# Kernel tuning notes

Measured on AMD Instinct MI355X. Metric: run time of the kernel, lower is better.

Reference implementation:

```python
import jax, jax.numpy as jnp
import numpy as np

THRESH = 0.9   # config['thresh_cnn']
R = 2          # config['radius'] -> maxpool kernel 2R+1=5, stride 1, padding R


def setup_inputs() -> dict:
    key = jax.random.key(0)
    # [B=1, C=1, D=64, H=512, W=512]
    pred_vol = jax.random.uniform(key, (1, 1, 64, 512, 512), dtype=jnp.float32)
    return {"pred_vol": pred_vol}


def reference(pred_vol):
    # threshold: keep values > thresh, else 0
    pred_thresh = jnp.where(pred_vol > THRESH, pred_vol, 0.0)
    # 3D max-pool, kernel 2R+1, stride 1, padding R (torch pads with -inf for maxpool)
    k = 2 * R + 1
    mp = jax.lax.reduce_window(
        pred_thresh, -jnp.inf, jax.lax.max,
        window_dimensions=(1, 1, k, k, k),
        window_strides=(1, 1, 1, 1, 1),
        padding=[(0, 0), (0, 0), (R, R), (R, R), (R, R)],
    )
    # keep only strict local maxima of the thresholded volume
    conf_vol = jnp.where((mp > 0.0) & (mp == pred_thresh), mp, 0.0)
    return jnp.squeeze(conf_vol)  # [D, H, W] dense peak confidence map
```

## Files before the change

kernel.cpp:

```cpp
#include <hip/hip_runtime.h>


#define THRESH 0.9f

constexpr int D = 64, H = 512, W = 512;
constexpr int TW = 64;
constexpr int TH = 16;
constexpr int DCHUNK = 16;
constexpr int HALO = 2;
constexpr int LROWS = TH + 2 * HALO;
constexpr int RAWQ  = TW / 4 + 2;
constexpr int RAWQ_S = RAWQ + 1;
constexpr int WMQ   = TW / 4;
constexpr int WMQ_S = WMQ + 1;

__device__ __forceinline__ float4 thresh4(float4 v) {
    v.x = (v.x > THRESH) ? v.x : 0.f;
    v.y = (v.y > THRESH) ? v.y : 0.f;
    v.z = (v.z > THRESH) ? v.z : 0.f;
    v.w = (v.w > THRESH) ? v.w : 0.f;
    return v;
}

__device__ __forceinline__ float4 max4(float4 a, float4 b) {
    return make_float4(fmaxf(a.x, b.x), fmaxf(a.y, b.y),
                       fmaxf(a.z, b.z), fmaxf(a.w, b.w));
}

__device__ __forceinline__ float4 wmax5(float4 a, float4 b, float4 c) {
    const float f2 = a.z, f3 = a.w, f4 = b.x, f5 = b.y, f6 = b.z, f7 = b.w;
    const float f8 = c.x, f9 = c.y;
    const float m45 = fmaxf(f4, f5);
    const float m56 = fmaxf(f5, f6);
    const float m345 = fmaxf(f3, m45);
    const float m456 = fmaxf(f4, m56);
    const float m567 = fmaxf(m56, f7);
    const float m678 = fmaxf(fmaxf(f6, f7), f8);
    float4 r;
    r.x = fmaxf(fmaxf(f2, f6), m345);
    r.y = fmaxf(fmaxf(f3, f7), m456);
    r.z = fmaxf(fmaxf(f4, f8), m567);
    r.w = fmaxf(fmaxf(f5, f9), m678);
    return r;
}

__global__ __launch_bounds__(256)
void peak3d_kernel(const float* __restrict__ in, float* __restrict__ out) {
    __shared__ float4 raw[LROWS * RAWQ_S];
    __shared__ float4 wmax[LROWS * WMQ_S];

    const int tx = threadIdx.x;
    const int ty = threadIdx.y;
    const int tid = ty * 16 + tx;

    const int w0 = blockIdx.x * TW;
    const int h0 = blockIdx.y * TH;
    const int d0 = blockIdx.z * DCHUNK;

    const int q0 = tid;
    const int q1 = tid + 256;
    const int r0 = q0 / RAWQ, c0 = q0 % RAWQ;
    const int r1 = q1 / RAWQ, c1 = q1 % RAWQ;
    const int lds0 = r0 * RAWQ_S + c0;
    const int lds1 = r1 * RAWQ_S + c1;
    const int gh0 = h0 + r0 - HALO, gw0 = w0 + 4 * c0 - 4;
    const int gh1 = h0 + r1 - HALO, gw1 = w0 + 4 * c1 - 4;
    const bool has1 = (q1 < LROWS * RAWQ);
    const bool ib0 = (gh0 >= 0 && gh0 < H && gw0 >= 0 && gw0 < W);
    const bool ib1 = has1 && (gh1 >= 0 && gh1 < H && gw1 >= 0 && gw1 < W);
    const size_t off0 = ib0 ? ((size_t)gh0 * W + gw0) : 0;
    const size_t off1 = ib1 ? ((size_t)gh1 * W + gw1) : 0;

    const float4 zero4 = make_float4(0.f, 0.f, 0.f, 0.f);
    float4 win[5], cen[5];
#pragma unroll
    for (int k = 0; k < 5; ++k) { win[k] = zero4; cen[k] = zero4; }

    auto loadSlice = [&](int dd, float4& p0, float4& p1) {
        p0 = zero4; p1 = zero4;
        if (dd >= 0 && dd < D) {
            const size_t base = (size_t)dd * (H * W);
            if (ib0) p0 = thresh4(*reinterpret_cast<const float4*>(in + base + off0));
            if (ib1) p1 = thresh4(*reinterpret_cast<const float4*>(in + base + off1));
        }
    };

    float4 p0, p1;
    loadSlice(d0 - HALO, p0, p1);

    for (int j = 0; j < 4; ++j) {
#pragma unroll
        for (int k = 0; k < 5; ++k) {
            const int s = 5 * j + k;
            const int ds = d0 - HALO + s;

            raw[lds0] = p0;
            if (has1) raw[lds1] = p1;
            if (s + 1 < DCHUNK + 2 * HALO) loadSlice(ds + 1, p0, p1);
            __syncthreads();

            const float4 tc = raw[(ty + HALO) * RAWQ_S + (tx + 1)];

            {
                int m = tid;
#pragma unroll
                for (int pass = 0; pass < 2; ++pass) {
                    if (m < LROWS * WMQ) {
                        const int r = m / WMQ, c = m % WMQ;
                        const float4* rp = &raw[r * RAWQ_S + c];
                        wmax[r * WMQ_S + c] = wmax5(rp[0], rp[1], rp[2]);
                    }
                    m += 256;
                }
            }
            __syncthreads();

            const float4* wp = &wmax[ty * WMQ_S + tx];
            float4 hv = wp[0];
            hv = max4(hv, wp[1 * WMQ_S]);
            hv = max4(hv, wp[2 * WMQ_S]);
            hv = max4(hv, wp[3 * WMQ_S]);
            hv = max4(hv, wp[4 * WMQ_S]);

            win[k] = hv;
            cen[k] = tc;

            if (s >= 4) {
                const int dout = ds - HALO;
                const float4 mp = max4(max4(max4(win[0], win[1]),
                                            max4(win[2], win[3])), win[4]);
                const float4 tcc = cen[(k + 3) % 5];
                float4 res;
                res.x = (mp.x > 0.f && mp.x == tcc.x) ? mp.x : 0.f;
                res.y = (mp.y > 0.f && mp.y == tcc.y) ? mp.y : 0.f;
                res.z = (mp.z > 0.f && mp.z == tcc.z) ? mp.z : 0.f;
                res.w = (mp.w > 0.f && mp.w == tcc.w) ? mp.w : 0.f;
                *reinterpret_cast<float4*>(
                    out + (size_t)dout * (H * W) + (size_t)(h0 + ty) * W + (w0 + 4 * tx)) = res;
            }
        }
    }
}

extern "C" void kernel_launch(void* const* d_in, const int* in_sizes, int n_in,
                              void* d_out, int out_size, void* d_ws, size_t ws_size,
                              hipStream_t stream) {
    const float* in = (const float*)d_in[0];
    float* out = (float*)d_out;
    dim3 grid(W / TW, H / TH, D / DCHUNK);
    dim3 block(16, 16, 1);
    hipLaunchKernelGGL(peak3d_kernel, grid, block, 0, stream, in, out);
}
```

Before: 133.1 us.

## Double-buffer LDS stages to drop a barrier, halve depth chunk, nontemporal stores

After: 122.1 us. 1.09x faster.

```diff
diff --git a/kernel.cpp b/kernel.cpp
--- a/kernel.cpp
+++ b/kernel.cpp
@@ -6,13 +6,17 @@
 constexpr int D = 64, H = 512, W = 512;
 constexpr int TW = 64;
 constexpr int TH = 16;
-constexpr int DCHUNK = 16;
+constexpr int DCHUNK = 8;
 constexpr int HALO = 2;
 constexpr int LROWS = TH + 2 * HALO;
 constexpr int RAWQ  = TW / 4 + 2;
 constexpr int RAWQ_S = RAWQ + 1;
 constexpr int WMQ   = TW / 4;
 constexpr int WMQ_S = WMQ + 1;
+constexpr int NS = DCHUNK + 2 * HALO;
+constexpr int T_ITERS = NS + 1;
+
+typedef float floatx4 __attribute__((ext_vector_type(4)));
 
 __device__ __forceinline__ float4 thresh4(float4 v) {
     v.x = (v.x > THRESH) ? v.x : 0.f;
@@ -46,8 +50,8 @@
 
 __global__ __launch_bounds__(256)
 void peak3d_kernel(const float* __restrict__ in, float* __restrict__ out) {
-    __shared__ float4 raw[LROWS * RAWQ_S];
-    __shared__ float4 wmax[LROWS * WMQ_S];
+    __shared__ float4 raw[2][LROWS * RAWQ_S];
+    __shared__ float4 wm [2][LROWS * WMQ_S];
 
     const int tx = threadIdx.x;
     const int ty = threadIdx.y;
@@ -88,55 +92,57 @@
     float4 p0, p1;
     loadSlice(d0 - HALO, p0, p1);
 
-    for (int j = 0; j < 4; ++j) {
+    for (int jj = 0; jj < (T_ITERS + 4) / 5; ++jj) {
 #pragma unroll
         for (int k = 0; k < 5; ++k) {
-            const int s = 5 * j + k;
-            const int ds = d0 - HALO + s;
+            const int t = 5 * jj + k;
+            if (t < T_ITERS) {
+                const int buf = t & 1;
 
-            raw[lds0] = p0;
-            if (has1) raw[lds1] = p1;
-            if (s + 1 < DCHUNK + 2 * HALO) loadSlice(ds + 1, p0, p1);
-            __syncthreads();
+                if (t <= NS - 1) {
+                    raw[buf][lds0] = p0;
+                    if (has1) raw[buf][lds1] = p1;
+                }
+                if (t + 1 <= NS - 1) loadSlice(d0 - HALO + t + 1, p0, p1);
 
-            const float4 tc = raw[(ty + HALO) * RAWQ_S + (tx + 1)];
+                __syncthreads();
 
-            {
-                int m = tid;
-#pragma unroll
-                for (int pass = 0; pass < 2; ++pass) {
-                    if (m < LROWS * WMQ) {
-                        const int r = m / WMQ, c = m % WMQ;
-                        const float4* rp = &raw[r * RAWQ_S + c];
-                        wmax[r * WMQ_S + c] = wmax5(rp[0], rp[1], rp[2]);
+                if (t <= NS - 1) {
+                    const float4* rp = &raw[buf][ty * RAWQ_S + tx];
+                    wm[buf][ty * WMQ_S + tx] = wmax5(rp[0], rp[1], rp[2]);
+                    if (tid < (LROWS - TH) * WMQ) {
+                        const int r = TH + (tid >> 4), c = tid & 15;
+                        const float4* rq = &raw[buf][r * RAWQ_S + c];
+                        wm[buf][r * WMQ_S + c] = wmax5(rq[0], rq[1], rq[2]);
                     }
-                    m += 256;
+                    cen[k] = raw[buf][(ty + HALO) * RAWQ_S + (tx + 1)];
                 }
-            }
-            __syncthreads();
 
-            const float4* wp = &wmax[ty * WMQ_S + tx];
-            float4 hv = wp[0];
-            hv = max4(hv, wp[1 * WMQ_S]);
-            hv = max4(hv, wp[2 * WMQ_S]);
-            hv = max4(hv, wp[3 * WMQ_S]);
-            hv = max4(hv, wp[4 * WMQ_S]);
+                if (t >= 1) {
+                    const float4* wp = &wm[buf ^ 1][ty * WMQ_S + tx];
+                    float4 hv = wp[0];
+                    hv = max4(hv, wp[1 * WMQ_S]);
+                    hv = max4(hv, wp[2 * WMQ_S]);
+                    hv = max4(hv, wp[3 * WMQ_S]);
+                    hv = max4(hv, wp[4 * WMQ_S]);
+                    win[(k + 4) % 5] = hv;
 
-            win[k] = hv;
-            cen[k] = tc;
-
-            if (s >= 4) {
-                const int dout = ds - HALO;
-                const float4 mp = max4(max4(max4(win[0], win[1]),
-                                            max4(win[2], win[3])), win[4]);
-                const float4 tcc = cen[(k + 3) % 5];
-                float4 res;
-                res.x = (mp.x > 0.f && mp.x == tcc.x) ? mp.x : 0.f;
-                res.y = (mp.y > 0.f && mp.y == tcc.y) ? mp.y : 0.f;
-                res.z = (mp.z > 0.f && mp.z == tcc.z) ? mp.z : 0.f;
-                res.w = (mp.w > 0.f && mp.w == tcc.w) ? mp.w : 0.f;
-                *reinterpret_cast<float4*>(
-                    out + (size_t)dout * (H * W) + (size_t)(h0 + ty) * W + (w0 + 4 * tx)) = res;
+                    if (t >= 5) {
+                        const int dout = d0 + (t - 5);
+                        const float4 mp = max4(max4(max4(win[0], win[1]),
+                                                    max4(win[2], win[3])), win[4]);
+                        const float4 tcc = cen[(k + 2) % 5];
+                        floatx4 res;
+                        res.x = (mp.x > 0.f && mp.x == tcc.x) ? mp.x : 0.f;
+                        res.y = (mp.y > 0.f && mp.y == tcc.y) ? mp.y : 0.f;
+                        res.z = (mp.z > 0.f && mp.z == tcc.z) ? mp.z : 0.f;
+                        res.w = (mp.w > 0.f && mp.w == tcc.w) ? mp.w : 0.f;
+                        floatx4* op = reinterpret_cast<floatx4*>(
+                            out + (size_t)dout * (H * W) +
+                            (size_t)(h0 + ty) * W + (w0 + 4 * tx));
+                        __builtin_nontemporal_store(res, op);
+                    }
+                }
             }
         }
     }
```

## Replace LDS tiling with per-wavefront register sweep using depth-max loads and shuffles

Applied to the files above, without the earlier changes.

After: 132.7 us. Within noise of the previous version (-0.3%).

```diff
diff --git a/kernel.cpp b/kernel.cpp
--- a/kernel.cpp
+++ b/kernel.cpp
@@ -4,15 +4,11 @@
 #define THRESH 0.9f
 
 constexpr int D = 64, H = 512, W = 512;
-constexpr int TW = 64;
-constexpr int TH = 16;
-constexpr int DCHUNK = 16;
-constexpr int HALO = 2;
-constexpr int LROWS = TH + 2 * HALO;
-constexpr int RAWQ  = TW / 4 + 2;
-constexpr int RAWQ_S = RAWQ + 1;
-constexpr int WMQ   = TW / 4;
-constexpr int WMQ_S = WMQ + 1;
+constexpr int HW = H * W;
+constexpr int HS = 8;
+constexpr int STEPS = HS + 4;
+
+typedef float floatx4 __attribute__((ext_vector_type(4)));
 
 __device__ __forceinline__ float4 thresh4(float4 v) {
     v.x = (v.x > THRESH) ? v.x : 0.f;
@@ -27,9 +23,9 @@
                        fmaxf(a.z, b.z), fmaxf(a.w, b.w));
 }
 
-__device__ __forceinline__ float4 wmax5(float4 a, float4 b, float4 c) {
-    const float f2 = a.z, f3 = a.w, f4 = b.x, f5 = b.y, f6 = b.z, f7 = b.w;
-    const float f8 = c.x, f9 = c.y;
+__device__ __forceinline__ float4 wmax5s(float f2, float f3, float4 b,
+                                         float f8, float f9) {
+    const float f4 = b.x, f5 = b.y, f6 = b.z, f7 = b.w;
     const float m45 = fmaxf(f4, f5);
     const float m56 = fmaxf(f5, f6);
     const float m345 = fmaxf(f3, m45);
@@ -46,98 +42,95 @@
 
 __global__ __launch_bounds__(256)
 void peak3d_kernel(const float* __restrict__ in, float* __restrict__ out) {
-    __shared__ float4 raw[LROWS * RAWQ_S];
-    __shared__ float4 wmax[LROWS * WMQ_S];
+    const int lane = threadIdx.x & 63;
+    const int wv   = threadIdx.x >> 6;
 
-    const int tx = threadIdx.x;
-    const int ty = threadIdx.y;
-    const int tid = ty * 16 + tx;
-
-    const int w0 = blockIdx.x * TW;
-    const int h0 = blockIdx.y * TH;
-    const int d0 = blockIdx.z * DCHUNK;
-
-    const int q0 = tid;
-    const int q1 = tid + 256;
-    const int r0 = q0 / RAWQ, c0 = q0 % RAWQ;
-    const int r1 = q1 / RAWQ, c1 = q1 % RAWQ;
-    const int lds0 = r0 * RAWQ_S + c0;
-    const int lds1 = r1 * RAWQ_S + c1;
-    const int gh0 = h0 + r0 - HALO, gw0 = w0 + 4 * c0 - 4;
-    const int gh1 = h0 + r1 - HALO, gw1 = w0 + 4 * c1 - 4;
-    const bool has1 = (q1 < LROWS * RAWQ);
-    const bool ib0 = (gh0 >= 0 && gh0 < H && gw0 >= 0 && gw0 < W);
-    const bool ib1 = has1 && (gh1 >= 0 && gh1 < H && gw1 >= 0 && gw1 < W);
-    const size_t off0 = ib0 ? ((size_t)gh0 * W + gw0) : 0;
-    const size_t off1 = ib1 ? ((size_t)gh1 * W + gw1) : 0;
+    const int task = blockIdx.x * 4 + wv;
+    const int d    = task >> 6;
+    const int h0   = (task & 63) * HS;
 
     const float4 zero4 = make_float4(0.f, 0.f, 0.f, 0.f);
-    float4 win[5], cen[5];
+
+    const float* pj[5];
+    bool dv[5];
 #pragma unroll
-    for (int k = 0; k < 5; ++k) { win[k] = zero4; cen[k] = zero4; }
+    for (int j = 0; j < 5; ++j) {
+        const int dz = d - 2 + j;
+        dv[j] = (dz >= 0 && dz < D);
+        pj[j] = in + (size_t)(dv[j] ? dz : 0) * HW;
+    }
 
-    auto loadSlice = [&](int dd, float4& p0, float4& p1) {
-        p0 = zero4; p1 = zero4;
-        if (dd >= 0 && dd < D) {
-            const size_t base = (size_t)dd * (H * W);
-            if (ib0) p0 = thresh4(*reinterpret_cast<const float4*>(in + base + off0));
-            if (ib1) p1 = thresh4(*reinterpret_cast<const float4*>(in + base + off1));
+    auto loadRow = [&](int r, float4& zA, float4& zB, float4& cA, float4& cB) {
+        zA = zero4; zB = zero4; cA = zero4; cB = zero4;
+        if (r >= 0 && r < H) {
+#pragma unroll
+            for (int j = 0; j < 5; ++j) {
+                if (dv[j]) {
+                    const float* p = pj[j] + (size_t)r * W + 4 * lane;
+                    const float4 a = thresh4(*reinterpret_cast<const float4*>(p));
+                    const float4 b = thresh4(*reinterpret_cast<const float4*>(p + 256));
+                    zA = max4(zA, a); zB = max4(zB, b);
+                    if (j == 2) { cA = a; cB = b; }
+                }
+            }
         }
     };
 
-    float4 p0, p1;
-    loadSlice(d0 - HALO, p0, p1);
+    float4 pzA, pzB, pcA, pcB;
+    loadRow(h0 - 2, pzA, pzB, pcA, pcB);
 
-    for (int j = 0; j < 4; ++j) {
+    float4 wza[5], wzb[5];
+    float4 cena[3], cenb[3];
 #pragma unroll
-        for (int k = 0; k < 5; ++k) {
-            const int s = 5 * j + k;
-            const int ds = d0 - HALO + s;
+    for (int k = 0; k < 5; ++k) { wza[k] = zero4; wzb[k] = zero4; }
+#pragma unroll
+    for (int k = 0; k < 3; ++k) { cena[k] = zero4; cenb[k] = zero4; }
 
-            raw[lds0] = p0;
-            if (has1) raw[lds1] = p1;
-            if (s + 1 < DCHUNK + 2 * HALO) loadSlice(ds + 1, p0, p1);
-            __syncthreads();
+#pragma unroll
+    for (int t = 0; t < STEPS; ++t) {
+        const float4 za = pzA, zb = pzB;
+        cena[t % 3] = pcA;
+        cenb[t % 3] = pcB;
+        if (t + 1 < STEPS) loadRow(h0 - 1 + t, pzA, pzB, pcA, pcB);
 
-            const float4 tc = raw[(ty + HALO) * RAWQ_S + (tx + 1)];
+        float f2a = __shfl_up(za.z, 1);
+        float f3a = __shfl_up(za.w, 1);
+        float f8a = __shfl_down(za.x, 1);
+        float f9a = __shfl_down(za.y, 1);
+        float f2b = __shfl_up(zb.z, 1);
+        float f3b = __shfl_up(zb.w, 1);
+        float f8b = __shfl_down(zb.x, 1);
+        float f9b = __shfl_down(zb.y, 1);
+        const float zb0x  = __shfl(zb.x, 0);
+        const float zb0y  = __shfl(zb.y, 0);
+        const float za63z = __shfl(za.z, 63);
+        const float za63w = __shfl(za.w, 63);
+        if (lane == 0)  { f2a = 0.f; f3a = 0.f; f2b = za63z; f3b = za63w; }
+        if (lane == 63) { f8a = zb0x; f9a = zb0y; f8b = 0.f; f9b = 0.f; }
 
-            {
-                int m = tid;
-#pragma unroll
-                for (int pass = 0; pass < 2; ++pass) {
-                    if (m < LROWS * WMQ) {
-                        const int r = m / WMQ, c = m % WMQ;
-                        const float4* rp = &raw[r * RAWQ_S + c];
-                        wmax[r * WMQ_S + c] = wmax5(rp[0], rp[1], rp[2]);
-                    }
-                    m += 256;
-                }
-            }
-            __syncthreads();
+        wza[t % 5] = wmax5s(f2a, f3a, za, f8a, f9a);
+        wzb[t % 5] = wmax5s(f2b, f3b, zb, f8b, f9b);
 
-            const float4* wp = &wmax[ty * WMQ_S + tx];
-            float4 hv = wp[0];
-            hv = max4(hv, wp[1 * WMQ_S]);
-            hv = max4(hv, wp[2 * WMQ_S]);
-            hv = max4(hv, wp[3 * WMQ_S]);
-            hv = max4(hv, wp[4 * WMQ_S]);
-
-            win[k] = hv;
-            cen[k] = tc;
-
-            if (s >= 4) {
-                const int dout = ds - HALO;
-                const float4 mp = max4(max4(max4(win[0], win[1]),
-                                            max4(win[2], win[3])), win[4]);
-                const float4 tcc = cen[(k + 3) % 5];
-                float4 res;
-                res.x = (mp.x > 0.f && mp.x == tcc.x) ? mp.x : 0.f;
-                res.y = (mp.y > 0.f && mp.y == tcc.y) ? mp.y : 0.f;
-                res.z = (mp.z > 0.f && mp.z == tcc.z) ? mp.z : 0.f;
-                res.w = (mp.w > 0.f && mp.w == tcc.w) ? mp.w : 0.f;
-                *reinterpret_cast<float4*>(
-                    out + (size_t)dout * (H * W) + (size_t)(h0 + ty) * W + (w0 + 4 * tx)) = res;
-            }
+        if (t >= 4) {
+            const int hout = h0 + t - 4;
+            const float4 mpa = max4(max4(max4(wza[0], wza[1]),
+                                         max4(wza[2], wza[3])), wza[4]);
+            const float4 mpb = max4(max4(max4(wzb[0], wzb[1]),
+                                         max4(wzb[2], wzb[3])), wzb[4]);
+            const float4 tca = cena[(t + 1) % 3];
+            const float4 tcb = cenb[(t + 1) % 3];
+            floatx4 ra, rc;
+            ra.x = (mpa.x > 0.f && mpa.x == tca.x) ? mpa.x : 0.f;
+            ra.y = (mpa.y > 0.f && mpa.y == tca.y) ? mpa.y : 0.f;
+            ra.z = (mpa.z > 0.f && mpa.z == tca.z) ? mpa.z : 0.f;
+            ra.w = (mpa.w > 0.f && mpa.w == tca.w) ? mpa.w : 0.f;
+            rc.x = (mpb.x > 0.f && mpb.x == tcb.x) ? mpb.x : 0.f;
+            rc.y = (mpb.y > 0.f && mpb.y == tcb.y) ? mpb.y : 0.f;
+            rc.z = (mpb.z > 0.f && mpb.z == tcb.z) ? mpb.z : 0.f;
+            rc.w = (mpb.w > 0.f && mpb.w == tcb.w) ? mpb.w : 0.f;
+            float* o = out + (size_t)d * HW + (size_t)hout * W + 4 * lane;
+            __builtin_nontemporal_store(ra, reinterpret_cast<floatx4*>(o));
+            __builtin_nontemporal_store(rc, reinterpret_cast<floatx4*>(o + 256));
         }
     }
 }
@@ -147,7 +140,7 @@
                               hipStream_t stream) {
     const float* in = (const float*)d_in[0];
     float* out = (float*)d_out;
-    dim3 grid(W / TW, H / TH, D / DCHUNK);
-    dim3 block(16, 16, 1);
+    dim3 grid(1024, 1, 1);
+    dim3 block(256, 1, 1);
     hipLaunchKernelGGL(peak3d_kernel, grid, block, 0, stream, in, out);
 }
```
